# Kernel optimization log

Hardware: AMD Instinct MI355X
Metric: run time of the kernel (lower is better)

## Reference

```python
import jax, jax.numpy as jnp
import numpy as np

D_MODEL = 1024
N_HEADS = 16
HEAD_DIM = D_MODEL // N_HEADS
SEQ = 2048
BATCH = 2
ROPE_BASE = 10000.0


def rope_cos_sin(seq_len, dim, dtype=jnp.float32):
    inv_freq = 1.0 / (ROPE_BASE ** (jnp.arange(0, dim, 2, dtype=jnp.float32) / dim))
    pos = jnp.arange(seq_len, dtype=jnp.float32)
    freqs = jnp.outer(pos, inv_freq)              # [S, dim/2]
    emb = jnp.concatenate([freqs, freqs], axis=-1)  # [S, dim]
    return jnp.cos(emb).astype(dtype), jnp.sin(emb).astype(dtype)


def rotate_half(x):
    x1, x2 = jnp.split(x, 2, axis=-1)
    return jnp.concatenate([-x2, x1], axis=-1)


def setup_inputs() -> dict:
    key = jax.random.key(0)
    kx, kq, kk, kv, ko = jax.random.split(key, 5)
    x = jax.random.normal(kx, (BATCH, SEQ, D_MODEL), dtype=jnp.float32)
    # causal boolean mask, broadcastable to [B, H, S, S]
    attn_mask = jnp.tril(jnp.ones((SEQ, SEQ), dtype=bool))[None, None]
    s = 1.0 / np.sqrt(D_MODEL)
    Wq = jax.random.normal(kq, (D_MODEL, D_MODEL), dtype=jnp.float32) * s
    Wk = jax.random.normal(kk, (D_MODEL, D_MODEL), dtype=jnp.float32) * s
    Wv = jax.random.normal(kv, (D_MODEL, D_MODEL), dtype=jnp.float32) * s
    Wo = jax.random.normal(ko, (D_MODEL, D_MODEL), dtype=jnp.float32) * s
    return {"x": x, "attn_mask": attn_mask, "Wq": Wq, "Wk": Wk, "Wv": Wv, "Wo": Wo}


def reference(x, attn_mask, Wq, Wk, Wv, Wo):
    B, S, _ = x.shape
    dtype = x.dtype
    # projections (nn.Linear: x @ W.T)
    def split_heads(t):
        return t.reshape(B, S, N_HEADS, HEAD_DIM).transpose(0, 2, 1, 3)  # [B,H,S,Dh]
    q = split_heads(x @ Wq.T)
    k = split_heads(x @ Wk.T)
    v = split_heads(x @ Wv.T)
    # RoPE
    cos, sin = rope_cos_sin(S, HEAD_DIM, dtype)  # [S, Dh]
    cos = cos[None, None]
    sin = sin[None, None]
    q = q * cos + rotate_half(q) * sin
    k = k * cos + rotate_half(k) * sin
    # float mask: 0 where True, finfo.min where False
    neg = jnp.finfo(dtype).min
    float_mask = jnp.where(attn_mask, jnp.zeros((), dtype), jnp.full((), neg, dtype))
    # scaled dot product attention
    scale = 1.0 / np.sqrt(HEAD_DIM)
    scores = jnp.einsum("bhqd,bhkd->bhqk", q, k) * scale + float_mask
    attn = jax.nn.softmax(scores, axis=-1)
    out = jnp.einsum("bhqk,bhkd->bhqd", attn, v)  # [B,H,S,Dh]
    out = out.transpose(0, 2, 1, 3).reshape(B, S, D_MODEL)
    return out @ Wo.T
```

## Files before the change

kernel.cpp:

```cpp
#include <hip/hip_runtime.h>
#include <hip/hip_bf16.h>
#include <math.h>

typedef unsigned short ushort_t;
typedef __attribute__((ext_vector_type(8))) short short8;
typedef __attribute__((ext_vector_type(4))) float f32x4;

#define D_MODEL 1024
#define SEQ     2048
#define NH      16
#define HD      64
#define BATCH   2
#define M_TOTAL (BATCH * SEQ)
#define SCL     0.18033688f
#define HSZ     4194304

__device__ __forceinline__ ushort_t f2bf(float f) {
    __hip_bfloat16 h = __float2bfloat16(f);
    ushort_t u;
    __builtin_memcpy(&u, &h, 2);
    return u;
}
__device__ __forceinline__ unsigned pack2(float a, float b) {
    __hip_bfloat162 h = __float22bfloat162_rn(make_float2(a, b));
    unsigned u;
    __builtin_memcpy(&u, &h, 4);
    return u;
}
__device__ __forceinline__ float fexp2(float x) { return __builtin_amdgcn_exp2f(x); }

typedef const __attribute__((address_space(1))) void* gp_t;
typedef __attribute__((address_space(3))) void* lp_t;
__device__ __forceinline__ void cp16(const void* g, void* l) {
    __builtin_amdgcn_global_load_lds((gp_t)g, (lp_t)l, 16, 0, 0);
}

__global__ __launch_bounds__(256) void prep(
    const float* __restrict__ x,
    const float* __restrict__ w0, const float* __restrict__ w1,
    const float* __restrict__ w2, const float* __restrict__ w3,
    ushort_t* __restrict__ xb, ushort_t* __restrict__ wb,
    float2* __restrict__ tab)
{
    int bid = blockIdx.x;
    if (bid < 4096) {
        size_t e = ((size_t)bid * 256 + threadIdx.x) * 8;
        const float* src;
        ushort_t* dst;
        size_t off;
        if (e < (size_t)HSZ) {
            src = x; dst = xb; off = e;
        } else {
            size_t r = e - HSZ;
            int j = (int)(r >> 20);
            off = r & 1048575u;
            src = (j == 0) ? w0 : (j == 1) ? w1 : (j == 2) ? w2 : w3;
            dst = wb + ((size_t)j << 20);
        }
        float4 a = *(const float4*)&src[off];
        float4 b = *(const float4*)&src[off + 4];
        uint4 u;
        u.x = pack2(a.x, a.y);
        u.y = pack2(a.z, a.w);
        u.z = pack2(b.x, b.y);
        u.w = pack2(b.z, b.w);
        *(uint4*)&dst[off] = u;
    } else {
        int idx = (bid - 4096) * 256 + threadIdx.x;
        int i = idx & 31, s = idx >> 5;
        float invf = powf(10000.0f, -(float)(2 * i) * (1.0f / 64.0f));
        float fr = (float)s * invf;
        float sn, cs;
        sincosf(fr, &sn, &cs);
        tab[idx] = make_float2(cs, sn);
    }
}

template <int OMODE>
__global__ __launch_bounds__(256) void gemm_k(
    const ushort_t* __restrict__ A,
    const ushort_t* __restrict__ W0, const ushort_t* __restrict__ W1,
    const ushort_t* __restrict__ W2,
    void* __restrict__ D0v, void* __restrict__ D1v, void* __restrict__ D2v,
    const float2* __restrict__ tab)
{
    __shared__ ushort_t As[128 * 64];
    __shared__ ushort_t Bs[128 * 64];
    const int K = D_MODEL;
    const int t = threadIdx.x;
    const int l = t & 63, w = t >> 6;
    const int wm = (w & 1) * 64, wn = (w >> 1) * 64;
    const int r15 = l & 15, q4 = l >> 4;

    const int bid = blockIdx.x;
    const int xcd = bid & 7, loc = bid >> 3;
    const int mt = (xcd >> 1) * 8 + (loc & 7);
    int nt, z;
    if (OMODE == 0) {
        int rest = loc >> 3;
        nt = (xcd & 1) * 4 + (rest & 3);
        z  = rest >> 2;
    } else {
        nt = (xcd & 1) * 4 + (loc >> 3);
        z  = 0;
    }
    const int m0 = mt * 128, n0 = nt * 128;
    const ushort_t* Wp = (z == 0) ? W0 : (z == 1 ? W1 : W2);
    void* Dp           = (z == 0) ? D0v : (z == 1 ? D1v : D2v);

    f32x4 acc[4][4];
#pragma unroll
    for (int i = 0; i < 4; ++i)
#pragma unroll
        for (int j = 0; j < 4; ++j) acc[i][j] = (f32x4){0.f, 0.f, 0.f, 0.f};

    for (int k0 = 0; k0 < K; k0 += 64) {
        __syncthreads();
#pragma unroll
        for (int p = 0; p < 4; ++p) {
            int idx = t + p * 256;
            int row = idx >> 3, c = idx & 7;
            int cs = c ^ (row & 7);
            cp16(&A [(size_t)(m0 + row) * K + k0 + cs * 8], &As[idx * 8]);
            cp16(&Wp[(size_t)(n0 + row) * K + k0 + cs * 8], &Bs[idx * 8]);
        }
        __syncthreads();
#pragma unroll
        for (int kk = 0; kk < 2; ++kk) {
            short8 af[4], bfr[4];
#pragma unroll
            for (int i = 0; i < 4; ++i) {
                int R = wm + 16 * i + r15;
                af[i] = *(const short8*)&As[R * 64 + (((kk * 4 + q4) ^ (R & 7))) * 8];
            }
#pragma unroll
            for (int j = 0; j < 4; ++j) {
                int R = wn + 16 * j + r15;
                bfr[j] = *(const short8*)&Bs[R * 64 + (((kk * 4 + q4) ^ (R & 7))) * 8];
            }
#pragma unroll
            for (int i = 0; i < 4; ++i)
#pragma unroll
                for (int j = 0; j < 4; ++j)
                    acc[i][j] = __builtin_amdgcn_mfma_f32_16x16x32_bf16(
                        af[i], bfr[j], acc[i][j], 0, 0, 0);
        }
    }

    if (OMODE == 1) {
        float* Dst = (float*)Dp;
#pragma unroll
        for (int i = 0; i < 4; ++i)
#pragma unroll
            for (int j = 0; j < 4; ++j)
#pragma unroll
                for (int r = 0; r < 4; ++r) {
                    int row = m0 + wm + 16 * i + q4 * 4 + r;
                    int col = n0 + wn + 16 * j + r15;
                    Dst[(size_t)row * D_MODEL + col] = acc[i][j][r];
                }
    } else if (z < 2) {
        ushort_t* Dst = (ushort_t*)Dp;
        const float scl = (z == 0) ? SCL : 1.0f;
#pragma unroll
        for (int i = 0; i < 4; ++i) {
#pragma unroll
            for (int r = 0; r < 4; ++r) {
                int row = m0 + wm + 16 * i + q4 * 4 + r;
                int b = row >> 11, s = row & (SEQ - 1);
                const float2* trow = &tab[s * 32];
#pragma unroll
                for (int j = 0; j < 2; ++j) {
                    int col = n0 + wn + 16 * j + r15;
                    int h = col >> 6, f = 16 * j + r15;
                    float2 csn = trow[f];
                    float cs = csn.x * scl, sn = csn.y * scl;
                    float lo = acc[i][j][r], hi = acc[i][j + 2][r];
                    size_t o = (((size_t)(b * NH + h)) * SEQ + s) * HD + f;
                    Dst[o]      = f2bf(lo * cs - hi * sn);
                    Dst[o + 32] = f2bf(hi * cs + lo * sn);
                }
            }
        }
    } else {
        ushort_t* Dst = (ushort_t*)Dp;
#pragma unroll
        for (int i = 0; i < 4; ++i)
#pragma unroll
            for (int j = 0; j < 4; ++j)
#pragma unroll
                for (int r = 0; r < 4; ++r) {
                    int row = m0 + wm + 16 * i + q4 * 4 + r;
                    int col = n0 + wn + 16 * j + r15;
                    int b = row >> 11, s = row & (SEQ - 1);
                    int h = col >> 6, d = col & (HD - 1);
                    size_t o = (((size_t)(b * NH + h)) * HD + d) * SEQ + s;
                    Dst[o] = f2bf(acc[i][j][r]);
                }
    }
}

__global__ __launch_bounds__(256, 3) void attn_fused(
    const ushort_t* __restrict__ Qw, const ushort_t* __restrict__ Kw,
    const ushort_t* __restrict__ Vt, ushort_t* __restrict__ Ow)
{
    __shared__ __align__(16) ushort_t Kl[2][64 * 64];
    __shared__ __align__(16) ushort_t Vl[2][64 * 64];
    __shared__ __align__(16) ushort_t Ps[4][16 * 72];

    const int t = threadIdx.x;
    const int l = t & 63, w = t >> 6;
    const int r15 = l & 15, q4 = l >> 4;
    const int bid = blockIdx.x;
    const int loc = bid >> 3;
    const int bh  = (bid & 7) * 4 + (loc & 3);
    const int s   = 31 - (loc >> 2);
    const int m   = s * 4 + w;
    const size_t baseQK = (size_t)bh * SEQ * HD;
    const size_t baseV  = (size_t)bh * HD * SEQ;

    const int L0 = t, L1 = t + 256;
    const int r0 = L0 >> 3, c0 = (L0 & 7) ^ (r0 & 7);
    const int r1 = L1 >> 3, c1 = (L1 & 7) ^ (r1 & 7);

    const ushort_t* qp = &Qw[baseQK + (size_t)(m * 16 + r15) * HD + q4 * 8];
    short8 qf0 = *(const short8*)qp;
    short8 qf1 = *(const short8*)(qp + 32);

    f32x4 oacc[4];
    float part[4];
#pragma unroll
    for (int nb = 0; nb < 4; ++nb) oacc[nb] = (f32x4){0.f, 0.f, 0.f, 0.f};
#pragma unroll
    for (int r = 0; r < 4; ++r) part[r] = 0.f;

    const int ig0 = m * 16 + q4 * 4;
    ushort_t* ps = &Ps[w][0];

    auto stage = [&](int jt, int buf) {
        cp16(&Kw[baseQK + (size_t)(jt * 64 + r0) * HD + c0 * 8], &Kl[buf][L0 * 8]);
        cp16(&Kw[baseQK + (size_t)(jt * 64 + r1) * HD + c1 * 8], &Kl[buf][L1 * 8]);
        cp16(&Vt[baseV + (size_t)r0 * SEQ + jt * 64 + c0 * 8],   &Vl[buf][L0 * 8]);
        cp16(&Vt[baseV + (size_t)r1 * SEQ + jt * 64 + c1 * 8],   &Vl[buf][L1 * 8]);
    };

    auto process = [&](int jt, int buf) {
        f32x4 sc[4];
#pragma unroll
        for (int nb = 0; nb < 4; ++nb) {
            int R  = nb * 16 + r15;
            int a0 = R * 8 + (q4 ^ (R & 7));
            int a1 = R * 8 + ((q4 + 4) ^ (R & 7));
            short8 kb0 = *(const short8*)&Kl[buf][a0 * 8];
            short8 kb1 = *(const short8*)&Kl[buf][a1 * 8];
            f32x4 zz = (f32x4){0.f, 0.f, 0.f, 0.f};
            zz = __builtin_amdgcn_mfma_f32_16x16x32_bf16(qf0, kb0, zz, 0, 0, 0);
            sc[nb] = __builtin_amdgcn_mfma_f32_16x16x32_bf16(qf1, kb1, zz, 0, 0, 0);
        }
        const bool diag = (jt == s);
#pragma unroll
        for (int r = 0; r < 4; ++r) {
            float p0 = fexp2(sc[0][r]), p1 = fexp2(sc[1][r]);
            float p2 = fexp2(sc[2][r]), p3 = fexp2(sc[3][r]);
            if (diag) {
                int qg = ig0 + r, jb = jt * 64 + r15;
                p0 = (jb      <= qg) ? p0 : 0.f;
                p1 = (jb + 16 <= qg) ? p1 : 0.f;
                p2 = (jb + 32 <= qg) ? p2 : 0.f;
                p3 = (jb + 48 <= qg) ? p3 : 0.f;
            }
            part[r] += (p0 + p1) + (p2 + p3);
            int ro = (q4 * 4 + r) * 72 + r15;
            ps[ro]      = f2bf(p0);
            ps[ro + 16] = f2bf(p1);
            ps[ro + 32] = f2bf(p2);
            ps[ro + 48] = f2bf(p3);
        }
        short8 pf0 = *(const short8*)&ps[r15 * 72 + q4 * 8];
        short8 pf1 = *(const short8*)&ps[r15 * 72 + q4 * 8 + 32];
#pragma unroll
        for (int nb = 0; nb < 4; ++nb) {
            int R  = nb * 16 + r15;
            int a0 = R * 8 + (q4 ^ (R & 7));
            int a1 = R * 8 + ((q4 + 4) ^ (R & 7));
            short8 vb0 = *(const short8*)&Vl[buf][a0 * 8];
            short8 vb1 = *(const short8*)&Vl[buf][a1 * 8];
            f32x4 o = __builtin_amdgcn_mfma_f32_16x16x32_bf16(pf0, vb0, oacc[nb], 0, 0, 0);
            oacc[nb] = __builtin_amdgcn_mfma_f32_16x16x32_bf16(pf1, vb1, o, 0, 0, 0);
        }
    };

    stage(0, 0);
    for (int jt = 0; jt <= s; ++jt) {
        __syncthreads();
        if (jt < s) stage(jt + 1, (jt + 1) & 1);
        process(jt, jt & 1);
    }

    float lsum[4];
#pragma unroll
    for (int r = 0; r < 4; ++r) {
        float rs = part[r];
#pragma unroll
        for (int off = 1; off < 16; off <<= 1)
            rs += __shfl_xor(rs, off, 64);
        lsum[r] = 1.0f / rs;
    }

    const int b = bh >> 4, h = bh & 15;
#pragma unroll
    for (int nb = 0; nb < 4; ++nb) {
#pragma unroll
        for (int r = 0; r < 4; ++r) {
            int sg = m * 16 + q4 * 4 + r;
            int d  = nb * 16 + r15;
            Ow[((size_t)(b * SEQ + sg)) * D_MODEL + h * HD + d] =
                f2bf(oacc[nb][r] * lsum[r]);
        }
    }
}

extern "C" void kernel_launch(void* const* d_in, const int* in_sizes, int n_in,
                              void* d_out, int out_size, void* d_ws, size_t ws_size,
                              hipStream_t stream)
{
    const float* x  = (const float*)d_in[0];
    const float* Wq = (const float*)d_in[2];
    const float* Wk = (const float*)d_in[3];
    const float* Wv = (const float*)d_in[4];
    const float* Wo = (const float*)d_in[5];

    ushort_t* qw = (ushort_t*)d_ws;
    ushort_t* kw = qw + HSZ;
    ushort_t* vt = kw + HSZ;
    ushort_t* xb = vt + HSZ;
    ushort_t* aw = xb;
    ushort_t* wb = xb + HSZ;
    float2*  tab = (float2*)(wb + HSZ);

    prep<<<4096 + 256, 256, 0, stream>>>(x, Wq, Wk, Wv, Wo, xb, wb, tab);
    gemm_k<0><<<768, 256, 0, stream>>>(
        xb, wb, wb + (1 << 20), wb + (2 << 20), qw, kw, vt, tab);
    attn_fused<<<1024, 256, 0, stream>>>(qw, kw, vt, aw);
    gemm_k<1><<<256, 256, 0, stream>>>(
        aw, wb + (3 << 20), nullptr, nullptr,
        (float*)d_out, nullptr, nullptr, nullptr);
}
```

Before: 194.7 us.

## Double-buffer GEMM shared-memory tiles with K-step 32 and one barrier per step

The projection GEMM now keeps two shared-memory buffers of 128x32 bf16 tiles. It issues the global-to-LDS copies for the next K slice before running the MFMAs on the current one, which cuts barriers per step from two to one and hides load latency behind compute. The LDS swizzle changes to a rotation that fits the 4-chunk row width. In exchange there are twice as many loop iterations, each doing half the MFMA work. Correctness relies on cp16 completing before the next barrier.

```diff
diff --git a/kernel.cpp b/kernel.cpp
--- a/kernel.cpp
+++ b/kernel.cpp
@@ -84,8 +84,8 @@
     void* __restrict__ D0v, void* __restrict__ D1v, void* __restrict__ D2v,
     const float2* __restrict__ tab)
 {
-    __shared__ ushort_t As[128 * 64];
-    __shared__ ushort_t Bs[128 * 64];
+    __shared__ ushort_t As[2][128 * 32];
+    __shared__ ushort_t Bs[2][128 * 32];
     const int K = D_MODEL;
     const int t = threadIdx.x;
     const int l = t & 63, w = t >> 6;
@@ -114,37 +114,39 @@
 #pragma unroll
         for (int j = 0; j < 4; ++j) acc[i][j] = (f32x4){0.f, 0.f, 0.f, 0.f};
 
-    for (int k0 = 0; k0 < K; k0 += 64) {
+    const int i0 = t, i1 = t + 256;
+    const int ro0 = i0 >> 2, c0 = ((i0 & 3) - (ro0 >> 1)) & 3;
+    const int ro1 = i1 >> 2, c1 = ((i1 & 3) - (ro1 >> 1)) & 3;
+
+    auto stage = [&](int k0, int buf) {
+        cp16(&A [(size_t)(m0 + ro0) * K + k0 + c0 * 8], &As[buf][i0 * 8]);
+        cp16(&A [(size_t)(m0 + ro1) * K + k0 + c1 * 8], &As[buf][i1 * 8]);
+        cp16(&Wp[(size_t)(n0 + ro0) * K + k0 + c0 * 8], &Bs[buf][i0 * 8]);
+        cp16(&Wp[(size_t)(n0 + ro1) * K + k0 + c1 * 8], &Bs[buf][i1 * 8]);
+    };
+
+    stage(0, 0);
+    for (int ki = 0; ki < K / 32; ++ki) {
         __syncthreads();
-#pragma unroll
-        for (int p = 0; p < 4; ++p) {
-            int idx = t + p * 256;
-            int row = idx >> 3, c = idx & 7;
-            int cs = c ^ (row & 7);
-            cp16(&A [(size_t)(m0 + row) * K + k0 + cs * 8], &As[idx * 8]);
-            cp16(&Wp[(size_t)(n0 + row) * K + k0 + cs * 8], &Bs[idx * 8]);
-        }
-        __syncthreads();
-#pragma unroll
-        for (int kk = 0; kk < 2; ++kk) {
-            short8 af[4], bfr[4];
-#pragma unroll
-            for (int i = 0; i < 4; ++i) {
-                int R = wm + 16 * i + r15;
-                af[i] = *(const short8*)&As[R * 64 + (((kk * 4 + q4) ^ (R & 7))) * 8];
-            }
-#pragma unroll
-            for (int j = 0; j < 4; ++j) {
-                int R = wn + 16 * j + r15;
-                bfr[j] = *(const short8*)&Bs[R * 64 + (((kk * 4 + q4) ^ (R & 7))) * 8];
-            }
-#pragma unroll
-            for (int i = 0; i < 4; ++i)
-#pragma unroll
-                for (int j = 0; j < 4; ++j)
-                    acc[i][j] = __builtin_amdgcn_mfma_f32_16x16x32_bf16(
-                        af[i], bfr[j], acc[i][j], 0, 0, 0);
-        }
+        if (ki < K / 32 - 1) stage((ki + 1) * 32, (ki + 1) & 1);
+        const int buf = ki & 1;
+        short8 af[4], bfr[4];
+#pragma unroll
+        for (int i = 0; i < 4; ++i) {
+            int R = wm + 16 * i + r15;
+            af[i] = *(const short8*)&As[buf][(R * 4 + ((q4 + (R >> 1)) & 3)) * 8];
+        }
+#pragma unroll
+        for (int j = 0; j < 4; ++j) {
+            int R = wn + 16 * j + r15;
+            bfr[j] = *(const short8*)&Bs[buf][(R * 4 + ((q4 + (R >> 1)) & 3)) * 8];
+        }
+#pragma unroll
+        for (int i = 0; i < 4; ++i)
+#pragma unroll
+            for (int j = 0; j < 4; ++j)
+                acc[i][j] = __builtin_amdgcn_mfma_f32_16x16x32_bf16(
+                    af[i], bfr[j], acc[i][j], 0, 0, 0);
     }
 
     if (OMODE == 1) {
```

Measured after the change: 194.3 us. About the same (-0.2%).
